# Performance work log

Measured on AMD Instinct MI355X. Metric: run time of the kernel, lower is better.

The kernel has to match this reference:

```python
import jax, jax.numpy as jnp
import numpy as np

N_SPK, N_UTT, D = 1024, 32, 128
EPS = 1e-8  # matches F.cosine_similarity eps


def setup_inputs() -> dict:
    key = jax.random.key(0)
    emb = jax.random.normal(key, (N_SPK * N_UTT, D), dtype=jnp.float32)
    emb = emb / jnp.linalg.norm(emb, axis=-1, keepdims=True)  # L2-normalized per docstring
    return {
        "embeddings": emb,
        "w": jnp.asarray(10.0, dtype=jnp.float32),
        "b": jnp.asarray(-5.0, dtype=jnp.float32),
        "n_speakers": N_SPK,
        "n_utterances": N_UTT,
    }


def reference(embeddings, w, b, n_speakers, n_utterances):
    # [N, M, D]
    e = embeddings.reshape(n_speakers, n_utterances, -1)
    cent = e.mean(axis=1)  # [N, D] full centroids
    # exclusive centroids: mean over all utterances except i -> [N, M, D]
    cent_excl = (e.sum(axis=1, keepdims=True) - e) / (n_utterances - 1)

    e_n = jnp.maximum(jnp.linalg.norm(e, axis=-1), EPS)          # [N, M]
    c_n = jnp.maximum(jnp.linalg.norm(cent, axis=-1), EPS)       # [N]
    ce_n = jnp.maximum(jnp.linalg.norm(cent_excl, axis=-1), EPS) # [N, M]

    # cosine sim of every utterance vs every full centroid: [N, M, N]
    sim = jnp.einsum('nmd,kd->nmk', e, cent) / (e_n[:, :, None] * c_n[None, None, :])
    # own-speaker entry uses the exclusive centroid instead
    sim_own = jnp.sum(e * cent_excl, axis=-1) / (e_n * ce_n)     # [N, M]
    eye = jnp.eye(n_speakers, dtype=bool)[:, None, :]            # [N, 1, N]
    sim = jnp.where(eye, sim_own[:, :, None], sim)

    logits = (w * sim + b).reshape(n_speakers * n_utterances, n_speakers)
    targets = jnp.repeat(jnp.arange(n_speakers), n_utterances)
    logp = jax.nn.log_softmax(logits, axis=-1)
    loss = -jnp.take_along_axis(logp, targets[:, None], axis=-1).mean()
    return loss
```

## Files before the change

kernel.cpp:

```cpp
#include <hip/hip_runtime.h>
#include <math.h>

#define NSPK 1024
#define NUTT 32
#define DIM  128
#define NROWS (NSPK * NUTT)
#define EPS 1e-8f
#define LOG2E 1.44269504f

typedef __attribute__((ext_vector_type(8))) short short8;
typedef __attribute__((ext_vector_type(4))) float floatx4;

__device__ inline unsigned short f2bf(float f) {
  union { float f; unsigned u; } v; v.f = f;
  unsigned r = v.u + 0x7fffu + ((v.u >> 16) & 1u);
  return (unsigned short)(r >> 16);
}

__device__ __forceinline__ void gll16(const unsigned short* g, unsigned short* l) {
  __builtin_amdgcn_global_load_lds(
      (const __attribute__((address_space(1))) unsigned int*)g,
      (__attribute__((address_space(3))) unsigned int*)l, 16, 0, 0);
}

__global__ __launch_bounds__(256) void k1(const float* __restrict__ emb,
                                          const float* __restrict__ wp,
                                          const float* __restrict__ bp,
                                          unsigned short* __restrict__ centC,
                                          float* __restrict__ rs2g,
                                          float* __restrict__ eolg,
                                          float* __restrict__ olvg,
                                          float* __restrict__ out) {
  __shared__ __align__(16) float Sl[2 * 128];
  __shared__ float red[4];

  int b = blockIdx.x, t = threadIdx.x;
  float w = wp[0], bb = bp[0];
  float M = bb + fabsf(w);
  if (b == 0 && t == 0) out[0] = 0.f;

  int sp = t >> 7, d = t & 127;
  {
    const float* eb = emb + (size_t)(b * 2 + sp) * NUTT * DIM + d;
    float s = 0.f;
#pragma unroll
    for (int m = 0; m < NUTT; ++m) s += eb[m * DIM];
    Sl[sp * 128 + d] = s;
    float p = s * s;
#pragma unroll
    for (int mask = 1; mask < 64; mask <<= 1) p += __shfl_xor(p, mask, 64);
    if ((t & 63) == 0) red[t >> 6] = p;
  }
  __syncthreads();
  float ss0 = red[0] + red[1], ss1 = red[2] + red[3];

  {
    float ss = sp ? ss1 : ss0;
    float s = Sl[sp * 128 + d];
    float cn = fmaxf(sqrtf(ss) * (1.0f / NUTT), EPS);
    centC[(size_t)(d >> 3) * (NSPK * 8) + (size_t)(b * 2 + sp) * 8 + (d & 7)] =
        f2bf(s / (NUTT * cn));
  }

  {
    int row = t >> 2, sub = t & 3;
    int rsp = row >> 5;
    const float* er = emb + (size_t)(b * 64 + row) * DIM + sub * 32;
    const float* Srow = &Sl[rsp * 128 + sub * 32];
    float ee = 0.f, es = 0.f;
#pragma unroll
    for (int i = 0; i < 8; ++i) {
      float4 ev = *(const float4*)&er[i * 4];
      float4 sv = *(const float4*)&Srow[i * 4];
      ee += ev.x * ev.x + ev.y * ev.y + ev.z * ev.z + ev.w * ev.w;
      es += ev.x * sv.x + ev.y * sv.y + ev.z * sv.z + ev.w * sv.w;
    }
    ee += __shfl_xor(ee, 1, 64); es += __shfl_xor(es, 1, 64);
    ee += __shfl_xor(ee, 2, 64); es += __shfl_xor(es, 2, 64);
    if (sub == 0) {
      float ss = rsp ? ss1 : ss0;
      float en = fmaxf(sqrtf(ee), EPS);
      float dot_own = (es - ee) * (1.0f / (NUTT - 1));
      float ex2 = (ss - 2.f * es + ee) * (1.0f / ((NUTT - 1) * (NUTT - 1)));
      float cen = fmaxf(sqrtf(ex2), EPS);
      float ol = w * dot_own / (en * cen) + bb;
      int gr = b * 64 + row;
      olvg[gr] = ol;
      eolg[gr] = exp2f((ol - M) * LOG2E);
      rs2g[gr] = w * LOG2E / en;
    }
  }
}

__global__ __launch_bounds__(512, 4) void k2(const float* __restrict__ emb,
                                             const unsigned short* __restrict__ centC,
                                             const float* __restrict__ rs2g,
                                             const float* __restrict__ eolg,
                                             const float* __restrict__ olvg,
                                             const float* __restrict__ wp,
                                             const float* __restrict__ bp,
                                             float* __restrict__ out) {
  __shared__ __align__(16) unsigned short A[8192];
  __shared__ __align__(16) unsigned short Bb[2][8192];
  __shared__ __align__(16) float sPart[4][64];

  int b = blockIdx.x, t = threadIdx.x;
  int wid = t >> 6, lane = t & 63, lg = lane >> 4, lc = lane & 15;
  int rh = wid & 1, cg = wid >> 1;
  float w = wp[0], bb = bp[0];
  float M = bb + fabsf(w);
  float c2 = -fabsf(w) * LOG2E;

#pragma unroll
  for (int i = 0; i < 4; ++i) {
    int idx4 = t + 512 * i;
    int row = idx4 >> 5, d4 = (idx4 & 31) << 2;
    float4 v = *(const float4*)(emb + (size_t)b * 8192 + (size_t)idx4 * 4);
    ushort4 bv;
    bv.x = f2bf(v.x); bv.y = f2bf(v.y); bv.z = f2bf(v.z); bv.w = f2bf(v.w);
    int rb = row >> 4, lcA = row & 15, kc = d4 >> 3, half = (d4 >> 2) & 1;
    *(ushort4*)&A[(rb * 256 + kc * 16 + lcA) * 8 + half * 4] = bv;
  }

  {
    int region = wid >> 1;
#pragma unroll
    for (int i = 0; i < 2; ++i) {
      int ks = (wid & 1) * 2 + i;
      gll16(centC + ((size_t)(ks * 4 + lg) * NSPK + region * 16 + lc) * 8,
            &Bb[0][(region * 4 + ks) * 512]);
    }
  }

  __syncthreads();

  short8 af[2][4];
#pragma unroll
  for (int rt = 0; rt < 2; ++rt)
#pragma unroll
    for (int ks = 0; ks < 4; ++ks)
      af[rt][ks] = *(const short8*)&A[((rh * 2 + rt) * 256 + (ks * 4 + lg) * 16 + lc) * 8];

  float rsL[8], eolL[8];
#pragma unroll
  for (int rt = 0; rt < 2; ++rt) {
    float4 r4 = *(const float4*)&rs2g[b * 64 + rh * 32 + rt * 16 + lg * 4];
    float4 o4 = *(const float4*)&eolg[b * 64 + rh * 32 + rt * 16 + lg * 4];
    rsL[rt * 4 + 0] = r4.x; rsL[rt * 4 + 1] = r4.y; rsL[rt * 4 + 2] = r4.z; rsL[rt * 4 + 3] = r4.w;
    eolL[rt * 4 + 0] = o4.x; eolL[rt * 4 + 1] = o4.y; eolL[rt * 4 + 2] = o4.z; eolL[rt * 4 + 3] = o4.w;
  }

  float sAcc[8];
#pragma unroll
  for (int j = 0; j < 8; ++j) sAcc[j] = 0.f;

  int own = b * 2 + rh;

  for (int p = 0; p < 16; ++p) {
    if (p > 0) __syncthreads();
    if (p < 15) {
      int region = wid >> 1;
      unsigned short* lb = Bb[(p + 1) & 1];
#pragma unroll
      for (int i = 0; i < 2; ++i) {
        int ks = (wid & 1) * 2 + i;
        gll16(centC + ((size_t)(ks * 4 + lg) * NSPK + (p + 1) * 64 + region * 16 + lc) * 8,
              &lb[(region * 4 + ks) * 512]);
      }
    }

    const unsigned short* Bp = Bb[p & 1];
    short8 bf[4];
#pragma unroll
    for (int ks = 0; ks < 4; ++ks)
      bf[ks] = *(const short8*)&Bp[((cg * 4 + ks) * 64 + lane) * 8];

    floatx4 acc[2];
#pragma unroll
    for (int rt = 0; rt < 2; ++rt) acc[rt] = (floatx4){0.f, 0.f, 0.f, 0.f};
#pragma unroll
    for (int ks = 0; ks < 4; ++ks)
#pragma unroll
      for (int rt = 0; rt < 2; ++rt)
        acc[rt] = __builtin_amdgcn_mfma_f32_16x16x32_bf16(af[rt][ks], bf[ks], acc[rt], 0, 0, 0);

    int col = p * 64 + cg * 16 + lc;
    bool isown = (col == own);
#pragma unroll
    for (int rt = 0; rt < 2; ++rt)
#pragma unroll
      for (int reg = 0; reg < 4; ++reg) {
        float l2 = fmaf(rsL[rt * 4 + reg], acc[rt][reg], c2);
        float e = exp2f(l2);
        if (isown) e = eolL[rt * 4 + reg];
        sAcc[rt * 4 + reg] += e;
      }
  }

#pragma unroll
  for (int mask = 1; mask < 16; mask <<= 1)
#pragma unroll
    for (int j = 0; j < 8; ++j) sAcc[j] += __shfl_xor(sAcc[j], mask, 64);

  if (lc == 0)
#pragma unroll
    for (int rt = 0; rt < 2; ++rt)
#pragma unroll
      for (int reg = 0; reg < 4; ++reg)
        sPart[cg][rh * 32 + rt * 16 + lg * 4 + reg] = sAcc[rt * 4 + reg];
  __syncthreads();

  if (t < 64) {
    float st = sPart[0][t] + sPart[1][t] + sPart[2][t] + sPart[3][t];
    float lossr = M + logf(st) - olvg[b * 64 + t];
#pragma unroll
    for (int mask = 1; mask < 64; mask <<= 1) lossr += __shfl_xor(lossr, mask, 64);
    if (t == 0) atomicAdd(out, lossr * (1.0f / NROWS));
  }
}

extern "C" void kernel_launch(void* const* d_in, const int* in_sizes, int n_in,
                              void* d_out, int out_size, void* d_ws, size_t ws_size,
                              hipStream_t stream) {
  const float* emb = (const float*)d_in[0];
  const float* wp  = (const float*)d_in[1];
  const float* bp  = (const float*)d_in[2];

  char* ws = (char*)d_ws;
  unsigned short* centC = (unsigned short*)ws;
  float* rs2g = (float*)(ws + 262144);
  float* eolg = (float*)(ws + 262144 + 131072);
  float* olvg = (float*)(ws + 262144 + 262144);
  float* out = (float*)d_out;

  hipLaunchKernelGGL(k1, dim3(512), dim3(256), 0, stream,
                     emb, wp, bp, centC, rs2g, eolg, olvg, out);
  hipLaunchKernelGGL(k2, dim3(512), dim3(512), 0, stream,
                     emb, centC, rs2g, eolg, olvg, wp, bp, out);
}
```

Before: 97.68 us.

## Retile similarity GEMM to 128-row tiles split over column halves with bf16 pre-pack

k1 now also converts the embeddings to bf16 in MFMA-ready layout in workspace. k2 gives each block 128 rows against half of the centroid columns, loading A through async global-to-LDS copies. Per-row partial sums are accumulated with atomics, and a new k3 computes the log-sum-exp loss. This doubles the A reuse per centroid load and removes the fp32 conversion from k2. In exchange it adds an extra kernel launch, global atomics, the bf16 embedding write and read, and larger LDS use (launch bounds drop to 2 blocks).

Result: no change. 97.66 us (-0.0%).

```diff
diff --git a/kernel.cpp b/kernel.cpp
--- a/kernel.cpp
+++ b/kernel.cpp
@@ -30,6 +30,8 @@
                                           float* __restrict__ rs2g,
                                           float* __restrict__ eolg,
                                           float* __restrict__ olvg,
+                                          unsigned short* __restrict__ embBF,
+                                          float* __restrict__ sRow,
                                           float* __restrict__ out) {
   __shared__ __align__(16) float Sl[2 * 128];
   __shared__ float red[4];
@@ -38,6 +40,7 @@
   float w = wp[0], bb = bp[0];
   float M = bb + fabsf(w);
   if (b == 0 && t == 0) out[0] = 0.f;
+  if (t < 64) sRow[b * 64 + t] = 0.f;
 
   int sp = t >> 7, d = t & 127;
   {
@@ -90,48 +93,57 @@
       rs2g[gr] = w * LOG2E / en;
     }
   }
-}
-
-__global__ __launch_bounds__(512, 4) void k2(const float* __restrict__ emb,
+
+  {
+    int gtile = b >> 1;
+#pragma unroll
+    for (int i = 0; i < 8; ++i) {
+      int idx4 = t + 256 * i;
+      int row64 = idx4 >> 5, d4 = (idx4 & 31) << 2;
+      float4 v = *(const float4*)(emb + (size_t)b * 8192 + (size_t)idx4 * 4);
+      ushort4 bv;
+      bv.x = f2bf(v.x); bv.y = f2bf(v.y); bv.z = f2bf(v.z); bv.w = f2bf(v.w);
+      int rbl = (b & 1) * 4 + (row64 >> 4);
+      int lcA = row64 & 15, kc = d4 >> 3, half = (d4 >> 2) & 1;
+      *(ushort4*)&embBF[((((size_t)gtile * 8 + rbl) * 16 + kc) * 16 + lcA) * 8 + half * 4] = bv;
+    }
+  }
+}
+
+__global__ __launch_bounds__(512, 2) void k2(const unsigned short* __restrict__ embBF,
                                              const unsigned short* __restrict__ centC,
                                              const float* __restrict__ rs2g,
                                              const float* __restrict__ eolg,
-                                             const float* __restrict__ olvg,
                                              const float* __restrict__ wp,
                                              const float* __restrict__ bp,
-                                             float* __restrict__ out) {
-  __shared__ __align__(16) unsigned short A[8192];
+                                             float* __restrict__ sRow) {
+  __shared__ __align__(16) unsigned short A[16384];
   __shared__ __align__(16) unsigned short Bb[2][8192];
-  __shared__ __align__(16) float sPart[4][64];
+  __shared__ __align__(16) float sPart[8][32];
 
   int b = blockIdx.x, t = threadIdx.x;
+  int gtile = b >> 1, ch = b & 1;
   int wid = t >> 6, lane = t & 63, lg = lane >> 4, lc = lane & 15;
-  int rh = wid & 1, cg = wid >> 1;
+  int rq = wid >> 1, cw = wid & 1;
   float w = wp[0], bb = bp[0];
-  float M = bb + fabsf(w);
   float c2 = -fabsf(w) * LOG2E;
 
-#pragma unroll
-  for (int i = 0; i < 4; ++i) {
-    int idx4 = t + 512 * i;
-    int row = idx4 >> 5, d4 = (idx4 & 31) << 2;
-    float4 v = *(const float4*)(emb + (size_t)b * 8192 + (size_t)idx4 * 4);
-    ushort4 bv;
-    bv.x = f2bf(v.x); bv.y = f2bf(v.y); bv.z = f2bf(v.z); bv.w = f2bf(v.w);
-    int rb = row >> 4, lcA = row & 15, kc = d4 >> 3, half = (d4 >> 2) & 1;
-    *(ushort4*)&A[(rb * 256 + kc * 16 + lcA) * 8 + half * 4] = bv;
-  }
-
-  {
-    int region = wid >> 1;
+  {
+    const unsigned short* g = embBF + ((size_t)gtile * 2048 + wid * 64 + lane) * 8;
+#pragma unroll
+    for (int i = 0; i < 4; ++i)
+      gll16(g + (size_t)i * 512 * 8, &A[(wid * 64 + i * 512) * 8]);
+  }
+  int cgS = wid >> 1;
+  int colbase0 = ch * 512;
+  {
 #pragma unroll
     for (int i = 0; i < 2; ++i) {
       int ks = (wid & 1) * 2 + i;
-      gll16(centC + ((size_t)(ks * 4 + lg) * NSPK + region * 16 + lc) * 8,
-            &Bb[0][(region * 4 + ks) * 512]);
-    }
-  }
-
+      gll16(centC + ((size_t)(ks * 4 + lg) * NSPK + colbase0 + cgS * 16 + lc) * 8,
+            &Bb[0][(cgS * 4 + ks) * 512]);
+    }
+  }
   __syncthreads();
 
   short8 af[2][4];
@@ -139,83 +151,103 @@
   for (int rt = 0; rt < 2; ++rt)
 #pragma unroll
     for (int ks = 0; ks < 4; ++ks)
-      af[rt][ks] = *(const short8*)&A[((rh * 2 + rt) * 256 + (ks * 4 + lg) * 16 + lc) * 8];
+      af[rt][ks] = *(const short8*)&A[(((rq * 2 + rt) * 16 + ks * 4 + lg) * 16 + lc) * 8];
 
   float rsL[8], eolL[8];
 #pragma unroll
   for (int rt = 0; rt < 2; ++rt) {
-    float4 r4 = *(const float4*)&rs2g[b * 64 + rh * 32 + rt * 16 + lg * 4];
-    float4 o4 = *(const float4*)&eolg[b * 64 + rh * 32 + rt * 16 + lg * 4];
+    float4 r4 = *(const float4*)&rs2g[gtile * 128 + rq * 32 + rt * 16 + lg * 4];
+    float4 o4 = *(const float4*)&eolg[gtile * 128 + rq * 32 + rt * 16 + lg * 4];
     rsL[rt * 4 + 0] = r4.x; rsL[rt * 4 + 1] = r4.y; rsL[rt * 4 + 2] = r4.z; rsL[rt * 4 + 3] = r4.w;
     eolL[rt * 4 + 0] = o4.x; eolL[rt * 4 + 1] = o4.y; eolL[rt * 4 + 2] = o4.z; eolL[rt * 4 + 3] = o4.w;
   }
 
+  int own = gtile * 4 + rq;
   float sAcc[8];
 #pragma unroll
   for (int j = 0; j < 8; ++j) sAcc[j] = 0.f;
 
-  int own = b * 2 + rh;
-
-  for (int p = 0; p < 16; ++p) {
+  for (int p = 0; p < 8; ++p) {
     if (p > 0) __syncthreads();
-    if (p < 15) {
-      int region = wid >> 1;
+    if (p < 7) {
       unsigned short* lb = Bb[(p + 1) & 1];
 #pragma unroll
       for (int i = 0; i < 2; ++i) {
         int ks = (wid & 1) * 2 + i;
-        gll16(centC + ((size_t)(ks * 4 + lg) * NSPK + (p + 1) * 64 + region * 16 + lc) * 8,
-              &lb[(region * 4 + ks) * 512]);
+        gll16(centC + ((size_t)(ks * 4 + lg) * NSPK + colbase0 + (p + 1) * 64 + cgS * 16 + lc) * 8,
+              &lb[(cgS * 4 + ks) * 512]);
       }
     }
 
     const unsigned short* Bp = Bb[p & 1];
-    short8 bf[4];
-#pragma unroll
-    for (int ks = 0; ks < 4; ++ks)
-      bf[ks] = *(const short8*)&Bp[((cg * 4 + ks) * 64 + lane) * 8];
-
-    floatx4 acc[2];
-#pragma unroll
-    for (int rt = 0; rt < 2; ++rt) acc[rt] = (floatx4){0.f, 0.f, 0.f, 0.f};
-#pragma unroll
-    for (int ks = 0; ks < 4; ++ks)
+#pragma unroll
+    for (int ct = 0; ct < 2; ++ct) {
+      short8 bf[4];
+#pragma unroll
+      for (int ks = 0; ks < 4; ++ks)
+        bf[ks] = *(const short8*)&Bp[(((cw * 2 + ct) * 4 + ks) * 64 + lane) * 8];
+
+      floatx4 acc[2];
+#pragma unroll
+      for (int rt = 0; rt < 2; ++rt) acc[rt] = (floatx4){0.f, 0.f, 0.f, 0.f};
+#pragma unroll
+      for (int ks = 0; ks < 4; ++ks)
+#pragma unroll
+        for (int rt = 0; rt < 2; ++rt)
+          acc[rt] = __builtin_amdgcn_mfma_f32_16x16x32_bf16(af[rt][ks], bf[ks], acc[rt], 0, 0, 0);
+
+      int col = colbase0 + p * 64 + cw * 32 + ct * 16 + lc;
+      bool isown = (col == own);
 #pragma unroll
       for (int rt = 0; rt < 2; ++rt)
-        acc[rt] = __builtin_amdgcn_mfma_f32_16x16x32_bf16(af[rt][ks], bf[ks], acc[rt], 0, 0, 0);
-
-    int col = p * 64 + cg * 16 + lc;
-    bool isown = (col == own);
+#pragma unroll
+        for (int reg = 0; reg < 4; ++reg) {
+          float l2 = fmaf(rsL[rt * 4 + reg], acc[rt][reg], c2);
+          float e = exp2f(l2);
+          if (isown) e = eolL[rt * 4 + reg];
+          sAcc[rt * 4 + reg] += e;
+        }
+    }
+  }
+
+#pragma unroll
+  for (int mask = 1; mask < 16; mask <<= 1)
+#pragma unroll
+    for (int j = 0; j < 8; ++j) sAcc[j] += __shfl_xor(sAcc[j], mask, 64);
+
+  if (lc == 0)
 #pragma unroll
     for (int rt = 0; rt < 2; ++rt)
 #pragma unroll
-      for (int reg = 0; reg < 4; ++reg) {
-        float l2 = fmaf(rsL[rt * 4 + reg], acc[rt][reg], c2);
-        float e = exp2f(l2);
-        if (isown) e = eolL[rt * 4 + reg];
-        sAcc[rt * 4 + reg] += e;
-      }
-  }
-
-#pragma unroll
-  for (int mask = 1; mask < 16; mask <<= 1)
-#pragma unroll
-    for (int j = 0; j < 8; ++j) sAcc[j] += __shfl_xor(sAcc[j], mask, 64);
-
-  if (lc == 0)
-#pragma unroll
-    for (int rt = 0; rt < 2; ++rt)
-#pragma unroll
       for (int reg = 0; reg < 4; ++reg)
-        sPart[cg][rh * 32 + rt * 16 + lg * 4 + reg] = sAcc[rt * 4 + reg];
-  __syncthreads();
-
-  if (t < 64) {
-    float st = sPart[0][t] + sPart[1][t] + sPart[2][t] + sPart[3][t];
-    float lossr = M + logf(st) - olvg[b * 64 + t];
-#pragma unroll
-    for (int mask = 1; mask < 64; mask <<= 1) lossr += __shfl_xor(lossr, mask, 64);
-    if (t == 0) atomicAdd(out, lossr * (1.0f / NROWS));
+        sPart[rq * 2 + cw][rt * 16 + lg * 4 + reg] = sAcc[rt * 4 + reg];
+  __syncthreads();
+
+  if (t < 128) {
+    float v = sPart[(t >> 5) * 2 + 0][t & 31] + sPart[(t >> 5) * 2 + 1][t & 31];
+    atomicAdd(&sRow[gtile * 128 + t], v);
+  }
+}
+
+__global__ __launch_bounds__(512) void k3(const float* __restrict__ sRow,
+                                          const float* __restrict__ olvg,
+                                          const float* __restrict__ wp,
+                                          const float* __restrict__ bp,
+                                          float* __restrict__ out) {
+  __shared__ float red[8];
+  int t = threadIdx.x;
+  int r = blockIdx.x * 512 + t;
+  float M = bp[0] + fabsf(wp[0]);
+  float v = M + logf(sRow[r]) - olvg[r];
+#pragma unroll
+  for (int mask = 1; mask < 64; mask <<= 1) v += __shfl_xor(v, mask, 64);
+  if ((t & 63) == 0) red[t >> 6] = v;
+  __syncthreads();
+  if (t == 0) {
+    float s = 0.f;
+#pragma unroll
+    for (int i = 0; i < 8; ++i) s += red[i];
+    atomicAdd(out, s * (1.0f / NROWS));
   }
 }
 
@@ -229,12 +261,16 @@
   char* ws = (char*)d_ws;
   unsigned short* centC = (unsigned short*)ws;
   float* rs2g = (float*)(ws + 262144);
-  float* eolg = (float*)(ws + 262144 + 131072);
-  float* olvg = (float*)(ws + 262144 + 262144);
+  float* eolg = (float*)(ws + 393216);
+  float* olvg = (float*)(ws + 524288);
+  float* sRow = (float*)(ws + 655360);
+  unsigned short* embBF = (unsigned short*)(ws + 786432);
   float* out = (float*)d_out;
 
   hipLaunchKernelGGL(k1, dim3(512), dim3(256), 0, stream,
-                     emb, wp, bp, centC, rs2g, eolg, olvg, out);
+                     emb, wp, bp, centC, rs2g, eolg, olvg, embBF, sRow, out);
   hipLaunchKernelGGL(k2, dim3(512), dim3(512), 0, stream,
-                     emb, centC, rs2g, eolg, olvg, wp, bp, out);
-}
+                     embBF, centC, rs2g, eolg, wp, bp, sRow);
+  hipLaunchKernelGGL(k3, dim3(64), dim3(512), 0, stream,
+                     sRow, olvg, wp, bp, out);
+}
```
